# Performance work log

Hardware: AMD Instinct MI355X
Metric: run time of the kernel (lower is better)

Reference implementation:

```python
import jax, jax.numpy as jnp
import numpy as np

BS, QLEN, DIM, NHEADS, SEG = 2, 2048, 640, 8, 5
C = DIM // SEG * (SEG - 1)  # 512, channels kept after aggregator
AGG = DIM // SEG            # 128, aggregated channel slice


def setup_inputs() -> dict:
    key = jax.random.key(0)
    ks = jax.random.split(key, 12)
    s = 0.02
    return {
        "Q": jax.random.normal(ks[0], (BS, QLEN, DIM), jnp.float32),
        # Linear weights stored [in, out] so y = x @ W + b
        "W_Q": jax.random.normal(ks[1], (DIM, DIM), jnp.float32) * s,
        "b_Q": jnp.zeros((DIM,), jnp.float32),
        "W_K": jax.random.normal(ks[2], (DIM, DIM), jnp.float32) * s,
        "b_K": jnp.zeros((DIM,), jnp.float32),
        "W_V": jax.random.normal(ks[3], (DIM, DIM), jnp.float32) * s,
        "b_V": jnp.zeros((DIM,), jnp.float32),
        "W_pos": jax.random.uniform(ks[4], (QLEN, C), jnp.float32, -0.02, 0.02),
        "W_agg": jax.random.normal(ks[5], (AGG, AGG), jnp.float32) * s,
        "b_agg": jnp.zeros((AGG,), jnp.float32),
        "W_out": jax.random.normal(ks[6], (DIM, DIM), jnp.float32) * s,
        "b_out": jnp.zeros((DIM,), jnp.float32),
    }


def reference(Q, W_Q, b_Q, W_K, b_K, W_V, b_V, W_pos, W_agg, b_agg, W_out, b_out):
    bs, L, dim = Q.shape
    hd = C // NHEADS  # per-head dim after aggregation (64)
    # self-attention: K = V = Q
    q = Q @ W_Q + b_Q
    k = Q @ W_K + b_K
    v = Q @ W_V + b_V
    qkv = jnp.stack([q, k, v])  # [3, bs, L, dim]
    # Aggregator: keep first 4/5 channels per branch, aggregate last 1/5 across q/k/v
    x_main = qkv[..., :C]                                   # [3, bs, L, C]
    x_agg0 = jax.nn.gelu(qkv[..., C:].mean(0) @ W_agg + b_agg)  # [bs, L, AGG]
    # pos embedding add (dropout is identity at eval)
    q_s = (x_main[0] + W_pos).reshape(bs, L, NHEADS, hd).transpose(0, 2, 1, 3)  # [bs,H,L,hd]
    k_s = (x_main[1] + W_pos).reshape(bs, L, NHEADS, hd).transpose(0, 2, 3, 1)  # [bs,H,hd,L]
    v_s = (x_main[2] + W_pos).reshape(bs, L, NHEADS, hd).transpose(0, 2, 1, 3)  # [bs,H,L,hd]
    scale = (DIM // NHEADS) ** -0.5  # note: uses dim//n_heads (80), not post-agg head dim
    scores = jnp.einsum("bhqd,bhdk->bhqk", q_s, k_s) * scale  # [bs,H,L,L]
    attn = jax.nn.softmax(scores, axis=-1)
    out = jnp.einsum("bhqk,bhkd->bhqd", attn, v_s)             # [bs,H,L,hd]
    out = out.transpose(0, 2, 1, 3).reshape(bs, L, C)
    out = jnp.concatenate([out, x_agg0], axis=-1) @ W_out + b_out  # [bs,L,dim]
    return out, attn
```

## Files before the change

kernel.cpp:

```cpp
#include <hip/hip_runtime.h>
#include <cstdint>
#include <cstddef>

#define BSZ   2
#define QL    2048
#define DIMN  640
#define NH    8
#define CMAIN 512
#define AGGD  128
#define MROWS 4096
#define SCALE_QK 0.11180339887498948f

typedef __bf16 bf16;
typedef __bf16 bf16x8 __attribute__((ext_vector_type(8)));
typedef __bf16 bf16x4v __attribute__((ext_vector_type(4)));
typedef float  f32x4  __attribute__((ext_vector_type(4)));

typedef __attribute__((address_space(1))) const uint32_t GU32;
typedef __attribute__((address_space(3))) uint32_t LU32;
#define GLL(g, l) __builtin_amdgcn_global_load_lds((GU32*)(g), (LU32*)(l), 16, 0, 0)

static __device__ __forceinline__ f32x4 mfma16(bf16x8 a, bf16x8 b, f32x4 c) {
    return __builtin_amdgcn_mfma_f32_16x16x32_bf16(a, b, c, 0, 0, 0);
}

static __device__ __forceinline__ void waitbar() {
    asm volatile("s_waitcnt vmcnt(0)" ::: "memory");
    __builtin_amdgcn_s_barrier();
    asm volatile("" ::: "memory");
}

static __device__ __forceinline__ bf16x8 ldsfrag(const bf16* base, int row, int kbyte) {
    return *(const bf16x8*)((const char*)base + row * 128 + (kbyte ^ ((row & 7) << 4)));
}

template<int NCH>
static __device__ __forceinline__ void stage_rows(bf16* ldsbuf, const char* gbase,
                                                  int strideB, int tid) {
    const int w = tid >> 6, lane = tid & 63;
    #pragma unroll
    for (int i = 0; i < NCH / 256; ++i) {
        int c = i * 256 + w * 64 + lane;
        int r = c >> 3;
        int kb = ((c & 7) * 16) ^ ((r & 7) << 4);
        GLL(gbase + (size_t)r * strideB + kb,
            (char*)ldsbuf + (size_t)(i * 256 + w * 64) * 16);
    }
}

template<int MI>
static __device__ __forceinline__ void gemm_main(
    const bf16* __restrict__ A, const bf16* __restrict__ BT,
    int m0, int n0, bf16* lds, f32x4 acc[MI][4])
{
    const int tid = threadIdx.x;
    const int w = tid >> 6, lane = tid & 63;
    const int lr = lane & 15, lg = lane >> 4;
    const int wm = (w >> 1) * (MI * 16), wn = (w & 1) * 64;
    constexpr int ASZ = MI * 2048;
    constexpr int BUF = ASZ + 8192;

    stage_rows<MI * 256>(lds,   (const char*)(A + (size_t)m0 * 640), 1280, tid);
    stage_rows<1024>(lds + ASZ, (const char*)(BT + (size_t)n0 * 640), 1280, tid);
    int cur = 0;
    #pragma unroll 1
    for (int ch = 0; ch < 10; ++ch) {
        waitbar();
        if (ch < 9) {
            int kk = (ch + 1) * 64;
            bf16* nb = lds + (cur ^ 1) * BUF;
            stage_rows<MI * 256>(nb,   (const char*)(A + (size_t)m0 * 640 + kk), 1280, tid);
            stage_rows<1024>(nb + ASZ, (const char*)(BT + (size_t)n0 * 640 + kk), 1280, tid);
        }
        const bf16* cA = lds + cur * BUF;
        const bf16* cB = cA + ASZ;
        #pragma unroll
        for (int ks = 0; ks < 2; ++ks) {
            bf16x8 a[MI], b[4];
            #pragma unroll
            for (int i = 0; i < MI; ++i) a[i] = ldsfrag(cA, wm + i * 16 + lr, ks * 64 + lg * 16);
            #pragma unroll
            for (int i = 0; i < 4; ++i)  b[i] = ldsfrag(cB, wn + i * 16 + lr, ks * 64 + lg * 16);
            #pragma unroll
            for (int mi = 0; mi < MI; ++mi)
                #pragma unroll
                for (int ni = 0; ni < 4; ++ni)
                    acc[mi][ni] = mfma16(a[mi], b[ni], acc[mi][ni]);
        }
        cur ^= 1;
    }
}

__global__ void __launch_bounds__(256) k_split_q(const float* __restrict__ Q,
                                                 bf16* __restrict__ Qbf) {
    int i = blockIdx.x * 256 + threadIdx.x;
    float4 v = ((const float4*)Q)[i];
    bf16x4v hv;
    hv[0] = (bf16)v.x; hv[1] = (bf16)v.y; hv[2] = (bf16)v.z; hv[3] = (bf16)v.w;
    *(bf16x4v*)(Qbf + (size_t)i * 4) = hv;
}

__global__ void __launch_bounds__(256) k_prep_w(
    const float* __restrict__ WQ, const float* __restrict__ WK,
    const float* __restrict__ WV, const float* __restrict__ WO,
    bf16* __restrict__ BTqkv, bf16* __restrict__ BTout)
{
    __shared__ float tl[64][65];
    const int ty = blockIdx.x / 10, tx = blockIdx.x % 10;
    const int wsel = blockIdx.y;
    const float* W = (wsel == 0) ? WQ : (wsel == 1) ? WK : (wsel == 2) ? WV : WO;
    const int tid = threadIdx.x;
    const int rr = tid >> 4;
    const int cc = (tid & 15) * 4;
    #pragma unroll
    for (int i = 0; i < 4; ++i) {
        int k = tx * 64 + rr + i * 16;
        float4 v = *(const float4*)(W + (size_t)k * 640 + ty * 64 + cc);
        tl[cc + 0][rr + i * 16] = v.x;
        tl[cc + 1][rr + i * 16] = v.y;
        tl[cc + 2][rr + i * 16] = v.z;
        tl[cc + 3][rr + i * 16] = v.w;
    }
    __syncthreads();
    bf16* dst; int nbase;
    if (wsel < 3) { dst = BTqkv; nbase = wsel * 640 + ty * 64; }
    else          { dst = BTout; nbase = ty * 64; }
    const int nl0 = tid >> 4;
    const int kl = (tid & 15) * 4;
    #pragma unroll
    for (int i = 0; i < 4; ++i) {
        int nl = nl0 + i * 16;
        bf16x4v hv;
        #pragma unroll
        for (int j = 0; j < 4; ++j) hv[j] = (bf16)tl[nl][kl + j];
        *(bf16x4v*)(dst + (size_t)(nbase + nl) * 640 + tx * 64 + kl) = hv;
    }
}

__global__ void __launch_bounds__(256) k_gemm_qkv(
    const bf16* __restrict__ Qbf, const bf16* __restrict__ BT,
    const float* __restrict__ bQ, const float* __restrict__ bK, const float* __restrict__ bV,
    const float* __restrict__ Wpos,
    bf16* __restrict__ qsbuf, bf16* __restrict__ vsT, float* __restrict__ aggbuf)
{
    __shared__ __align__(16) bf16 lds[2 * (8192 + 8192)];
    const int m0 = blockIdx.x * 128, n0 = blockIdx.y * 128;
    f32x4 acc[4][4];
    {
        f32x4 z = {0.f, 0.f, 0.f, 0.f};
        #pragma unroll
        for (int mi = 0; mi < 4; ++mi)
            #pragma unroll
            for (int ni = 0; ni < 4; ++ni) acc[mi][ni] = z;
    }
    gemm_main<4>(Qbf, BT, m0, n0, lds, acc);

    const int tid = threadIdx.x, w = tid >> 6, lane = tid & 63;
    const int lr = lane & 15, lg = lane >> 4;
    const int wm = (w >> 1) * 64, wn = (w & 1) * 64;
    const int p = n0 / 640;
    const float* bias = (p == 0) ? bQ : (p == 1) ? bK : bV;

    #pragma unroll
    for (int mi = 0; mi < 4; ++mi)
        #pragma unroll
        for (int ni = 0; ni < 4; ++ni) {
            int n = n0 + wn + ni * 16 + lr;
            int c = n - p * 640;
            int rbase = m0 + wm + mi * 16 + lg * 4;
            float bval = bias[c];
            if (c < 512) {
                int hh = c >> 6, d = c & 63;
                #pragma unroll
                for (int r = 0; r < 4; ++r) {
                    int rg = rbase + r;
                    int bb = rg >> 11, l = rg & 2047;
                    float v = acc[mi][ni][r] + bval + Wpos[(size_t)l * 512 + c];
                    if (p < 2)
                        qsbuf[(((size_t)(p * 2 + bb) * 8 + hh) * 2048 + l) * 64 + d] = (bf16)v;
                    else
                        vsT[(((size_t)(bb * 8 + hh)) * 64 + d) * 2048 + l] = (bf16)v;
                }
            } else {
                int j = c - 512;
                #pragma unroll
                for (int r = 0; r < 4; ++r) {
                    int rg = rbase + r;
                    aggbuf[((size_t)p * MROWS + rg) * AGGD + j] = acc[mi][ni][r] + bval;
                }
            }
        }
}

__global__ void __launch_bounds__(256) k_agg(const float* __restrict__ aggbuf,
                                             const float* __restrict__ Wagg, const float* __restrict__ bagg,
                                             bf16* __restrict__ xcat)
{
    __shared__ float wl[128 * 128];
    __shared__ float xl[32 * 128];
    const int tid = threadIdx.x;
    const int r0 = blockIdx.x * 32;
    for (int i = tid; i < 128 * 128; i += 256) wl[i] = Wagg[i];
    for (int i = tid; i < 32 * 128; i += 256) {
        int row = i >> 7, j = i & 127;
        size_t rg = r0 + row;
        float s = aggbuf[rg * AGGD + j]
                + aggbuf[((size_t)MROWS + rg) * AGGD + j]
                + aggbuf[((size_t)2 * MROWS + rg) * AGGD + j];
        xl[i] = s * (1.0f / 3.0f);
    }
    __syncthreads();
    const int row = tid >> 3;
    const int jo0 = (tid & 7) * 16;
    float acc[16];
    #pragma unroll
    for (int jj = 0; jj < 16; ++jj) acc[jj] = 0.f;
    for (int j = 0; j < 128; ++j) {
        float xv = xl[row * 128 + j];
        const float* wr = &wl[j * 128 + jo0];
        #pragma unroll
        for (int jj = 0; jj < 16; ++jj) acc[jj] = fmaf(xv, wr[jj], acc[jj]);
    }
    size_t rg = r0 + row;
    #pragma unroll
    for (int jj = 0; jj < 16; ++jj) {
        float t = acc[jj] + bagg[jo0 + jj];
        float g = 0.5f * t * (1.0f + tanhf(0.7978845608028654f * (t + 0.044715f * t * t * t)));
        xcat[rg * 640 + 512 + jo0 + jj] = (bf16)g;
    }
}

__global__ void __launch_bounds__(256) k_attn(const bf16* __restrict__ qsbuf, const bf16* __restrict__ vsT,
                                              float* __restrict__ gattn,
                                              bf16* __restrict__ xcat)
{
    __shared__ __align__(16) bf16 smem[2][8192];
    __shared__ __align__(16) bf16 p_lds[4][16 * 64];

    const int bh = blockIdx.y;
    const int b = bh >> 3, h = bh & 7;
    const int q0 = blockIdx.x * 64;
    const int tid = threadIdx.x, w = tid >> 6, lane = tid & 63;
    const int lr = lane & 15, lg = lane >> 4;

    const bf16* qbase = qsbuf + (size_t)(b * 8 + h) * (2048 * 64);
    const bf16* kbase = qsbuf + (size_t)((2 + b) * 8 + h) * (2048 * 64);
    const bf16* vtb   = vsT + (size_t)(b * 8 + h) * (64 * 2048);

    bf16x8 aq[2];
    {
        const bf16* qp = qbase + (size_t)(q0 + w * 16 + lr) * 64 + lg * 8;
        aq[0] = *(const bf16x8*)(qp);
        aq[1] = *(const bf16x8*)(qp + 32);
    }

    float lsum[4] = {0.f, 0.f, 0.f, 0.f};
    stage_rows<1024>(smem[0], (const char*)kbase, 128, tid);
    int cur = 0;
    #pragma unroll 1
    for (int kt = 0; kt < 16; ++kt) {
        waitbar();
        if (kt < 15)
            stage_rows<1024>(smem[cur ^ 1], (const char*)kbase + (size_t)(kt + 1) * 16384, 128, tid);
        f32x4 s[8];
        {
            f32x4 z = {0.f, 0.f, 0.f, 0.f};
            #pragma unroll
            for (int ni = 0; ni < 8; ++ni) s[ni] = z;
        }
        #pragma unroll
        for (int ks = 0; ks < 2; ++ks)
            #pragma unroll
            for (int ni = 0; ni < 8; ++ni)
                s[ni] = mfma16(aq[ks], ldsfrag(smem[cur], ni * 16 + lr, ks * 64 + lg * 16), s[ni]);
        #pragma unroll
        for (int ni = 0; ni < 8; ++ni)
            #pragma unroll
            for (int r = 0; r < 4; ++r)
                lsum[r] += __expf(s[ni][r] * SCALE_QK);
        cur ^= 1;
    }
    float invl[4];
    #pragma unroll
    for (int r = 0; r < 4; ++r) {
        float t = lsum[r];
        t += __shfl_xor(t, 1);
        t += __shfl_xor(t, 2);
        t += __shfl_xor(t, 4);
        t += __shfl_xor(t, 8);
        invl[r] = 1.0f / t;
    }

    f32x4 o[4];
    {
        f32x4 z = {0.f, 0.f, 0.f, 0.f};
        #pragma unroll
        for (int ni = 0; ni < 4; ++ni) o[ni] = z;
    }
    float* attnrow = gattn + (size_t)bh * 2048 * 2048;

    stage_rows<512>(smem[0],        (const char*)kbase, 128, tid);
    stage_rows<512>(smem[0] + 4096, (const char*)vtb, 4096, tid);
    cur = 0;
    #pragma unroll 1
    for (int kt = 0; kt < 32; ++kt) {
        if (kt == 0) asm volatile("s_waitcnt vmcnt(0)" ::: "memory");
        else         asm volatile("s_waitcnt vmcnt(16)" ::: "memory");
        __builtin_amdgcn_s_barrier();
        asm volatile("" ::: "memory");
        if (kt < 31) {
            stage_rows<512>(smem[cur ^ 1],        (const char*)kbase + (size_t)(kt + 1) * 8192, 128, tid);
            stage_rows<512>(smem[cur ^ 1] + 4096, (const char*)vtb + (size_t)(kt + 1) * 128, 4096, tid);
        }
        __builtin_amdgcn_sched_barrier(0);
        const bf16* kb = smem[cur];
        const bf16* vb = smem[cur] + 4096;
        f32x4 s[4];
        {
            f32x4 z = {0.f, 0.f, 0.f, 0.f};
            #pragma unroll
            for (int ni = 0; ni < 4; ++ni) s[ni] = z;
        }
        #pragma unroll
        for (int ks = 0; ks < 2; ++ks)
            #pragma unroll
            for (int ni = 0; ni < 4; ++ni)
                s[ni] = mfma16(aq[ks], ldsfrag(kb, ni * 16 + lr, ks * 64 + lg * 16), s[ni]);
        #pragma unroll
        for (int ni = 0; ni < 4; ++ni) {
            #pragma unroll
            for (int r = 0; r < 4; ++r) {
                float pv = __expf(s[ni][r] * SCALE_QK) * invl[r];
                int qr = q0 + w * 16 + lg * 4 + r;
                attnrow[(size_t)qr * 2048 + kt * 64 + ni * 16 + lr] = pv;
                int prow = lg * 4 + r;
                int pb = prow * 128 + (((ni * 16 + lr) * 2) ^ ((prow & 7) << 4));
                *(bf16*)((char*)&p_lds[w][0] + pb) = (bf16)pv;
            }
        }
        #pragma unroll
        for (int ks = 0; ks < 2; ++ks) {
            bf16x8 pa = ldsfrag(&p_lds[w][0], lr, ks * 64 + lg * 16);
            #pragma unroll
            for (int ni = 0; ni < 4; ++ni)
                o[ni] = mfma16(pa, ldsfrag(vb, ni * 16 + lr, ks * 64 + lg * 16), o[ni]);
        }
        cur ^= 1;
    }

    #pragma unroll
    for (int ni = 0; ni < 4; ++ni) {
        #pragma unroll
        for (int r = 0; r < 4; ++r) {
            int qr = q0 + w * 16 + lg * 4 + r;
            size_t rg = (size_t)b * 2048 + qr;
            int c = h * 64 + ni * 16 + lr;
            xcat[rg * 640 + c] = (bf16)o[ni][r];
        }
    }
}

__global__ void __launch_bounds__(256) k_gemm_out(
    const bf16* __restrict__ X, const bf16* __restrict__ BT,
    const float* __restrict__ bout, float* __restrict__ out0)
{
    __shared__ __align__(16) bf16 lds[2 * (4096 + 8192)];
    const int m0 = blockIdx.x * 64, n0 = blockIdx.y * 128;
    f32x4 acc[2][4];
    {
        f32x4 z = {0.f, 0.f, 0.f, 0.f};
        #pragma unroll
        for (int mi = 0; mi < 2; ++mi)
            #pragma unroll
            for (int ni = 0; ni < 4; ++ni) acc[mi][ni] = z;
    }
    gemm_main<2>(X, BT, m0, n0, lds, acc);

    const int tid = threadIdx.x, w = tid >> 6, lane = tid & 63;
    const int lr = lane & 15, lg = lane >> 4;
    const int wm = (w >> 1) * 32, wn = (w & 1) * 64;
    #pragma unroll
    for (int mi = 0; mi < 2; ++mi)
        #pragma unroll
        for (int ni = 0; ni < 4; ++ni) {
            int n = n0 + wn + ni * 16 + lr;
            float bv = bout[n];
            #pragma unroll
            for (int r = 0; r < 4; ++r) {
                int rg = m0 + wm + mi * 16 + lg * 4 + r;
                out0[(size_t)rg * 640 + n] = acc[mi][ni][r] + bv;
            }
        }
}

extern "C" void kernel_launch(void* const* d_in, const int* in_sizes, int n_in,
                              void* d_out, int out_size, void* d_ws, size_t ws_size,
                              hipStream_t stream)
{
    (void)in_sizes; (void)n_in; (void)out_size; (void)ws_size;
    const float* Q    = (const float*)d_in[0];
    const float* WQ   = (const float*)d_in[1];
    const float* bQ   = (const float*)d_in[2];
    const float* WK   = (const float*)d_in[3];
    const float* bK   = (const float*)d_in[4];
    const float* WV   = (const float*)d_in[5];
    const float* bV   = (const float*)d_in[6];
    const float* Wpos = (const float*)d_in[7];
    const float* Wagg = (const float*)d_in[8];
    const float* bagg = (const float*)d_in[9];
    const float* WO   = (const float*)d_in[10];
    const float* bout = (const float*)d_in[11];

    float* out0  = (float*)d_out;
    float* gattn = out0 + (size_t)MROWS * DIMN;

    char* ws = (char*)d_ws;
    bf16* Qbf    = (bf16*)(ws);                 ws += (size_t)MROWS * DIMN * 2;
    bf16* BTqkv  = (bf16*)(ws);                 ws += (size_t)1920 * 640 * 2;
    bf16* BTout  = (bf16*)(ws);                 ws += (size_t)640 * 640 * 2;
    bf16* qsbuf  = (bf16*)(ws);                 ws += (size_t)4 * 8 * 2048 * 64 * 2;
    bf16* vsT    = (bf16*)(ws);                 ws += (size_t)16 * 64 * 2048 * 2;
    float* aggbuf= (float*)(ws);                ws += (size_t)3 * MROWS * AGGD * 4;
    bf16* xcat   = (bf16*)(ws);                 ws += (size_t)MROWS * DIMN * 2;

    k_split_q<<<dim3(2560), dim3(256), 0, stream>>>(Q, Qbf);
    k_prep_w<<<dim3(100, 4), dim3(256), 0, stream>>>(WQ, WK, WV, WO, BTqkv, BTout);
    k_gemm_qkv<<<dim3(32, 15), dim3(256), 0, stream>>>(Qbf, BTqkv,
                                                       bQ, bK, bV, Wpos, qsbuf, vsT, aggbuf);
    k_agg<<<dim3(128), dim3(256), 0, stream>>>(aggbuf, Wagg, bagg, xcat);
    k_attn<<<dim3(32, 16), dim3(256), 0, stream>>>(qsbuf, vsT, gattn, xcat);
    k_gemm_out<<<dim3(64, 5), dim3(256), 0, stream>>>(xcat, BTout, bout, out0);
}
```

Before: 168.0 us.

## Transpose QK MFMA operands for vectorized attn stores and widen key tiles

Swaps the MFMA operand order in the attention score computation so each lane holds four consecutive key columns of one query row. This allows 16-byte float4 stores of the full attention matrix and packed bf16x4 writes into the P staging buffer, instead of scalar strided stores. Softmax now uses exp2 with the log of the row sum folded into the exponent, which replaces the per-element multiply by the inverse sum. The second pass moves from 64-key to 128-key tiles, doubling LDS use per block and possibly lowering occupancy.

```diff
diff --git a/kernel.cpp b/kernel.cpp
--- a/kernel.cpp
+++ b/kernel.cpp
@@ -10,6 +10,7 @@
 #define AGGD  128
 #define MROWS 4096
 #define SCALE_QK 0.11180339887498948f
+#define C2EXP (SCALE_QK * 1.4426950408889634f)
 
 typedef __bf16 bf16;
 typedef __bf16 bf16x8 __attribute__((ext_vector_type(8)));
@@ -20,6 +21,9 @@
 typedef __attribute__((address_space(3))) uint32_t LU32;
 #define GLL(g, l) __builtin_amdgcn_global_load_lds((GU32*)(g), (LU32*)(l), 16, 0, 0)
 
+#define EXP2F(x) __builtin_amdgcn_exp2f(x)
+#define LOG2F(x) __builtin_amdgcn_logf(x)
+
 static __device__ __forceinline__ f32x4 mfma16(bf16x8 a, bf16x8 b, f32x4 c) {
     return __builtin_amdgcn_mfma_f32_16x16x32_bf16(a, b, c, 0, 0, 0);
 }
@@ -30,19 +34,20 @@
     asm volatile("" ::: "memory");
 }
 
-static __device__ __forceinline__ bf16x8 ldsfrag(const bf16* base, int row, int kbyte) {
-    return *(const bf16x8*)((const char*)base + row * 128 + (kbyte ^ ((row & 7) << 4)));
-}
-
-template<int NCH>
-static __device__ __forceinline__ void stage_rows(bf16* ldsbuf, const char* gbase,
-                                                  int strideB, int tid) {
+template<int ROWB>
+static __device__ __forceinline__ bf16x8 ldsfragR(const bf16* base, int row, int kbyte) {
+    return *(const bf16x8*)((const char*)base + row * ROWB + (kbyte ^ ((row & 7) << 4)));
+}
+
+template<int NCH, int ROWB>
+static __device__ __forceinline__ void stage_rowsR(bf16* ldsbuf, const char* gbase,
+                                                   int strideB, int tid) {
     const int w = tid >> 6, lane = tid & 63;
     #pragma unroll
     for (int i = 0; i < NCH / 256; ++i) {
         int c = i * 256 + w * 64 + lane;
-        int r = c >> 3;
-        int kb = ((c & 7) * 16) ^ ((r & 7) << 4);
+        int r = c / (ROWB / 16);
+        int kb = ((c % (ROWB / 16)) * 16) ^ ((r & 7) << 4);
         GLL(gbase + (size_t)r * strideB + kb,
             (char*)ldsbuf + (size_t)(i * 256 + w * 64) * 16);
     }
@@ -60,8 +65,8 @@
     constexpr int ASZ = MI * 2048;
     constexpr int BUF = ASZ + 8192;
 
-    stage_rows<MI * 256>(lds,   (const char*)(A + (size_t)m0 * 640), 1280, tid);
-    stage_rows<1024>(lds + ASZ, (const char*)(BT + (size_t)n0 * 640), 1280, tid);
+    stage_rowsR<MI * 256, 128>(lds,   (const char*)(A + (size_t)m0 * 640), 1280, tid);
+    stage_rowsR<1024, 128>(lds + ASZ, (const char*)(BT + (size_t)n0 * 640), 1280, tid);
     int cur = 0;
     #pragma unroll 1
     for (int ch = 0; ch < 10; ++ch) {
@@ -69,8 +74,8 @@
         if (ch < 9) {
             int kk = (ch + 1) * 64;
             bf16* nb = lds + (cur ^ 1) * BUF;
-            stage_rows<MI * 256>(nb,   (const char*)(A + (size_t)m0 * 640 + kk), 1280, tid);
-            stage_rows<1024>(nb + ASZ, (const char*)(BT + (size_t)n0 * 640 + kk), 1280, tid);
+            stage_rowsR<MI * 256, 128>(nb,   (const char*)(A + (size_t)m0 * 640 + kk), 1280, tid);
+            stage_rowsR<1024, 128>(nb + ASZ, (const char*)(BT + (size_t)n0 * 640 + kk), 1280, tid);
         }
         const bf16* cA = lds + cur * BUF;
         const bf16* cB = cA + ASZ;
@@ -78,9 +83,9 @@
         for (int ks = 0; ks < 2; ++ks) {
             bf16x8 a[MI], b[4];
             #pragma unroll
-            for (int i = 0; i < MI; ++i) a[i] = ldsfrag(cA, wm + i * 16 + lr, ks * 64 + lg * 16);
-            #pragma unroll
-            for (int i = 0; i < 4; ++i)  b[i] = ldsfrag(cB, wn + i * 16 + lr, ks * 64 + lg * 16);
+            for (int i = 0; i < MI; ++i) a[i] = ldsfragR<128>(cA, wm + i * 16 + lr, ks * 64 + lg * 16);
+            #pragma unroll
+            for (int i = 0; i < 4; ++i)  b[i] = ldsfragR<128>(cB, wn + i * 16 + lr, ks * 64 + lg * 16);
             #pragma unroll
             for (int mi = 0; mi < MI; ++mi)
                 #pragma unroll
@@ -234,8 +239,8 @@
                                               float* __restrict__ gattn,
                                               bf16* __restrict__ xcat)
 {
-    __shared__ __align__(16) bf16 smem[2][8192];
-    __shared__ __align__(16) bf16 p_lds[4][16 * 64];
+    __shared__ __align__(16) bf16 smem[2][16384];
+    __shared__ __align__(16) bf16 p_lds[4][16 * 128];
 
     const int bh = blockIdx.y;
     const int b = bh >> 3, h = bh & 7;
@@ -254,14 +259,16 @@
         aq[1] = *(const bf16x8*)(qp + 32);
     }
 
-    float lsum[4] = {0.f, 0.f, 0.f, 0.f};
-    stage_rows<1024>(smem[0], (const char*)kbase, 128, tid);
+    float lsum = 0.f;
+    stage_rowsR<1024, 128>(smem[0], (const char*)kbase, 128, tid);
     int cur = 0;
     #pragma unroll 1
     for (int kt = 0; kt < 16; ++kt) {
         waitbar();
         if (kt < 15)
-            stage_rows<1024>(smem[cur ^ 1], (const char*)kbase + (size_t)(kt + 1) * 16384, 128, tid);
+            stage_rowsR<1024, 128>(smem[cur ^ 1], (const char*)kbase + (size_t)(kt + 1) * 16384, 128, tid);
+        __builtin_amdgcn_sched_barrier(0);
+        const bf16* kb = smem[cur];
         f32x4 s[8];
         {
             f32x4 z = {0.f, 0.f, 0.f, 0.f};
@@ -272,24 +279,17 @@
         for (int ks = 0; ks < 2; ++ks)
             #pragma unroll
             for (int ni = 0; ni < 8; ++ni)
-                s[ni] = mfma16(aq[ks], ldsfrag(smem[cur], ni * 16 + lr, ks * 64 + lg * 16), s[ni]);
+                s[ni] = mfma16(ldsfragR<128>(kb, ni * 16 + lr, ks * 64 + lg * 16), aq[ks], s[ni]);
         #pragma unroll
         for (int ni = 0; ni < 8; ++ni)
             #pragma unroll
             for (int r = 0; r < 4; ++r)
-                lsum[r] += __expf(s[ni][r] * SCALE_QK);
+                lsum += EXP2F(s[ni][r] * C2EXP);
         cur ^= 1;
     }
-    float invl[4];
-    #pragma unroll
-    for (int r = 0; r < 4; ++r) {
-        float t = lsum[r];
-        t += __shfl_xor(t, 1);
-        t += __shfl_xor(t, 2);
-        t += __shfl_xor(t, 4);
-        t += __shfl_xor(t, 8);
-        invl[r] = 1.0f / t;
-    }
+    lsum += __shfl_xor(lsum, 16);
+    lsum += __shfl_xor(lsum, 32);
+    const float l2i = -LOG2F(lsum);
 
     f32x4 o[4];
     {
@@ -297,53 +297,54 @@
         #pragma unroll
         for (int ni = 0; ni < 4; ++ni) o[ni] = z;
     }
-    float* attnrow = gattn + (size_t)bh * 2048 * 2048;
-
-    stage_rows<512>(smem[0],        (const char*)kbase, 128, tid);
-    stage_rows<512>(smem[0] + 4096, (const char*)vtb, 4096, tid);
+    float* attnrow = gattn + (size_t)bh * 2048 * 2048 + (size_t)(q0 + w * 16 + lr) * 2048;
+
+    stage_rowsR<1024, 128>(smem[0],        (const char*)kbase, 128, tid);
+    stage_rowsR<1024, 256>(smem[0] + 8192, (const char*)vtb, 4096, tid);
     cur = 0;
     #pragma unroll 1
-    for (int kt = 0; kt < 32; ++kt) {
+    for (int kt = 0; kt < 16; ++kt) {
         if (kt == 0) asm volatile("s_waitcnt vmcnt(0)" ::: "memory");
-        else         asm volatile("s_waitcnt vmcnt(16)" ::: "memory");
+        else         asm volatile("s_waitcnt vmcnt(8)" ::: "memory");
         __builtin_amdgcn_s_barrier();
         asm volatile("" ::: "memory");
-        if (kt < 31) {
-            stage_rows<512>(smem[cur ^ 1],        (const char*)kbase + (size_t)(kt + 1) * 8192, 128, tid);
-            stage_rows<512>(smem[cur ^ 1] + 4096, (const char*)vtb + (size_t)(kt + 1) * 128, 4096, tid);
+        if (kt < 15) {
+            stage_rowsR<1024, 128>(smem[cur ^ 1],        (const char*)kbase + (size_t)(kt + 1) * 16384, 128, tid);
+            stage_rowsR<1024, 256>(smem[cur ^ 1] + 8192, (const char*)vtb + (size_t)(kt + 1) * 256, 4096, tid);
         }
         __builtin_amdgcn_sched_barrier(0);
         const bf16* kb = smem[cur];
-        const bf16* vb = smem[cur] + 4096;
-        f32x4 s[4];
+        const bf16* vb = smem[cur] + 8192;
+        f32x4 s[8];
         {
             f32x4 z = {0.f, 0.f, 0.f, 0.f};
             #pragma unroll
-            for (int ni = 0; ni < 4; ++ni) s[ni] = z;
+            for (int ni = 0; ni < 8; ++ni) s[ni] = z;
         }
         #pragma unroll
         for (int ks = 0; ks < 2; ++ks)
             #pragma unroll
+            for (int ni = 0; ni < 8; ++ni)
+                s[ni] = mfma16(ldsfragR<128>(kb, ni * 16 + lr, ks * 64 + lg * 16), aq[ks], s[ni]);
+        bf16* pl = &p_lds[w][0];
+        float* arow = attnrow + kt * 128;
+        #pragma unroll
+        for (int ni = 0; ni < 8; ++ni) {
+            f32x4 p;
+            #pragma unroll
+            for (int r = 0; r < 4; ++r) p[r] = EXP2F(fmaf(s[ni][r], C2EXP, l2i));
+            *(f32x4*)(arow + ni * 16 + lg * 4) = p;
+            bf16x4v pb;
+            #pragma unroll
+            for (int r = 0; r < 4; ++r) pb[r] = (bf16)p[r];
+            *(bf16x4v*)((char*)pl + lr * 256 + ((ni * 32 + lg * 8) ^ ((lr & 7) << 4))) = pb;
+        }
+        #pragma unroll
+        for (int ks = 0; ks < 4; ++ks) {
+            bf16x8 pa = ldsfragR<256>(pl, lr, ks * 64 + lg * 16);
+            #pragma unroll
             for (int ni = 0; ni < 4; ++ni)
-                s[ni] = mfma16(aq[ks], ldsfrag(kb, ni * 16 + lr, ks * 64 + lg * 16), s[ni]);
-        #pragma unroll
-        for (int ni = 0; ni < 4; ++ni) {
-            #pragma unroll
-            for (int r = 0; r < 4; ++r) {
-                float pv = __expf(s[ni][r] * SCALE_QK) * invl[r];
-                int qr = q0 + w * 16 + lg * 4 + r;
-                attnrow[(size_t)qr * 2048 + kt * 64 + ni * 16 + lr] = pv;
-                int prow = lg * 4 + r;
-                int pb = prow * 128 + (((ni * 16 + lr) * 2) ^ ((prow & 7) << 4));
-                *(bf16*)((char*)&p_lds[w][0] + pb) = (bf16)pv;
-            }
-        }
-        #pragma unroll
-        for (int ks = 0; ks < 2; ++ks) {
-            bf16x8 pa = ldsfrag(&p_lds[w][0], lr, ks * 64 + lg * 16);
-            #pragma unroll
-            for (int ni = 0; ni < 4; ++ni)
-                o[ni] = mfma16(pa, ldsfrag(vb, ni * 16 + lr, ks * 64 + lg * 16), o[ni]);
+                o[ni] = mfma16(pa, ldsfragR<256>(vb, ni * 16 + lr, ks * 64 + lg * 16), o[ni]);
         }
         cur ^= 1;
     }
```

Measured after the change: 157.9 us, median of 2. -6.0%, faster.
